# Kernel tuning notes

Hardware: AMD Instinct MI355X
Metric: run time of the kernel (lower is better)

Reference implementation:

```python
import jax, jax.numpy as jnp
import numpy as np

B, S, D = 1, 1024, 2048          # batch, seq, hidden
H, KH, HD = 16, 16, 128          # heads, kv heads, head_dim
E, K, FI = 8, 4, 1408            # experts, top_k, moe_intermediate
FS = 5632                        # shared expert intermediate
WIN = 512                        # sliding window
THETA = 1.0e6                    # rope base
EPS = 1e-6                       # rmsnorm eps


def setup_inputs() -> dict:
    key = jax.random.key(0)
    ks = jax.random.split(key, 16)
    nrm = lambda k, shape: jax.random.normal(k, shape, jnp.float32) * 0.02
    return dict(
        hidden_states=jax.random.normal(ks[0], (B, S, D), jnp.float32),
        ln1_w=jnp.ones((D,), jnp.float32),
        ln2_w=jnp.ones((D,), jnp.float32),
        wq=nrm(ks[1], (D, H * HD)), bq=jnp.zeros((H * HD,), jnp.float32),
        wk=nrm(ks[2], (D, KH * HD)), bk=jnp.zeros((KH * HD,), jnp.float32),
        wv=nrm(ks[3], (D, KH * HD)), bv=jnp.zeros((KH * HD,), jnp.float32),
        wo=nrm(ks[4], (H * HD, D)),
        w_router=nrm(ks[5], (D, E)),
        w_gate_e=nrm(ks[6], (E, D, FI)),
        w_up_e=nrm(ks[7], (E, D, FI)),
        w_down_e=nrm(ks[8], (E, FI, D)),
        ws_gate=nrm(ks[9], (D, FS)),
        ws_up=nrm(ks[10], (D, FS)),
        ws_down=nrm(ks[11], (FS, D)),
        w_shared_gate=nrm(ks[12], (D, 1)),
    )


def _rms(h, w):
    v = jnp.mean(h * h, axis=-1, keepdims=True)
    return h * jax.lax.rsqrt(v + EPS) * w


def _rope(q, k):
    pos = jnp.arange(S, dtype=jnp.float32)
    inv = 1.0 / (THETA ** (jnp.arange(0, HD, 2, dtype=jnp.float32) / HD))
    ang = pos[:, None] * inv[None, :]                      # [S, HD/2]
    cos = jnp.concatenate([jnp.cos(ang)] * 2, -1)[None, :, None, :]
    sin = jnp.concatenate([jnp.sin(ang)] * 2, -1)[None, :, None, :]
    rot = lambda t: jnp.concatenate([-t[..., HD // 2:], t[..., :HD // 2]], -1)
    return q * cos + rot(q) * sin, k * cos + rot(k) * sin


def reference(hidden_states, ln1_w, ln2_w, wq, bq, wk, bk, wv, bv, wo,
              w_router, w_gate_e, w_up_e, w_down_e,
              ws_gate, ws_up, ws_down, w_shared_gate):
    x = hidden_states
    # --- sliding-window causal attention ---
    h = _rms(x, ln1_w)
    q = (h @ wq + bq).reshape(B, S, H, HD)
    k = (h @ wk + bk).reshape(B, S, KH, HD)
    v = (h @ wv + bv).reshape(B, S, KH, HD)
    q, k = _rope(q, k)
    scores = jnp.einsum('bqhd,bkhd->bhqk', q, k) * (HD ** -0.5)
    i = jnp.arange(S)[:, None]
    j = jnp.arange(S)[None, :]
    mask = (j <= i) & (i - j < WIN)                        # causal + window
    scores = jnp.where(mask[None, None], scores, jnp.finfo(scores.dtype).min)
    attn = jax.nn.softmax(scores, axis=-1)
    o = jnp.einsum('bhqk,bkhd->bqhd', attn, v).reshape(B, S, H * HD) @ wo
    x = x + o
    # --- sparse MoE block ---
    h = _rms(x, ln2_w)
    t = h.reshape(B * S, D)
    logits = (t @ w_router).astype(jnp.float32)
    probs = jax.nn.softmax(logits, axis=-1)                # [T, E]
    top_w, top_i = jax.lax.top_k(probs, K)                 # norm_topk_prob=False
    cw = jnp.zeros((B * S, E), probs.dtype).at[jnp.arange(B * S)[:, None], top_i].set(top_w)
    # routed experts (dense combine == gather/dispatch/grouped-GEMM/combine)
    g = jnp.einsum('td,edf->etf', t, w_gate_e)
    u = jnp.einsum('td,edf->etf', t, w_up_e)
    eo = jnp.einsum('etf,efd->etd', jax.nn.silu(g) * u, w_down_e)
    routed = jnp.einsum('te,etd->td', cw, eo)
    # shared expert with sigmoid gate
    shared = (jax.nn.silu(t @ ws_gate) * (t @ ws_up)) @ ws_down
    sgate = jax.nn.sigmoid(t @ w_shared_gate)              # [T, 1]
    moe = routed + sgate * shared
    return x + moe.reshape(B, S, D)
```

## Files before the change

### kernel.cpp

```cpp
#include <hip/hip_runtime.h>

#define S_ 1024
#define D_ 2048
#define H_ 16
#define HD_ 128
#define E_ 8
#define FI_ 1408
#define FS_ 5632
#define WIN_ 512
#define T_ 1024
#define QKVN 6144

typedef _Float16 f16;
typedef __attribute__((ext_vector_type(8))) _Float16 f16x8;
typedef __attribute__((ext_vector_type(4))) _Float16 f16x4;
typedef __attribute__((ext_vector_type(4))) float f32x4;

#define MFMA16(a, b, c) __builtin_amdgcn_mfma_f32_16x16x32_f16((a), (b), (c), 0, 0, 0)

__device__ __forceinline__ void gload16(const void* g, void* l) {
    __builtin_amdgcn_global_load_lds(
        (const __attribute__((address_space(1))) unsigned*)g,
        (__attribute__((address_space(3))) unsigned*)l, 16, 0, 0);
}

__global__ __launch_bounds__(256) void rmsnorm16_kernel(const float* __restrict__ x,
                                                        const float* __restrict__ w,
                                                        f16* __restrict__ out) {
    int t = blockIdx.x;
    const float* xr = x + (long)t * D_;
    int base = threadIdx.x * 8;
    float4 v0 = *(const float4*)(xr + base);
    float4 v1 = *(const float4*)(xr + base + 4);
    float ss = v0.x*v0.x + v0.y*v0.y + v0.z*v0.z + v0.w*v0.w
             + v1.x*v1.x + v1.y*v1.y + v1.z*v1.z + v1.w*v1.w;
    #pragma unroll
    for (int off = 1; off < 64; off <<= 1) ss += __shfl_xor(ss, off);
    __shared__ float red[4];
    if ((threadIdx.x & 63) == 0) red[threadIdx.x >> 6] = ss;
    __syncthreads();
    float tot = red[0] + red[1] + red[2] + red[3];
    float scale = rsqrtf(tot / (float)D_ + 1e-6f);
    float4 w0 = *(const float4*)(w + base);
    float4 w1 = *(const float4*)(w + base + 4);
    f16x8 o;
    o[0] = (f16)(v0.x*scale*w0.x); o[1] = (f16)(v0.y*scale*w0.y);
    o[2] = (f16)(v0.z*scale*w0.z); o[3] = (f16)(v0.w*scale*w0.w);
    o[4] = (f16)(v1.x*scale*w1.x); o[5] = (f16)(v1.y*scale*w1.y);
    o[6] = (f16)(v1.z*scale*w1.z); o[7] = (f16)(v1.w*scale*w1.w);
    *(f16x8*)(out + (long)t * D_ + base) = o;
}

__global__ __launch_bounds__(256) void tconv_kernel(const float* __restrict__ src,
                                                    f16* __restrict__ dst,
                                                    int K, int N, long sSrc, long sDst,
                                                    int mode) {
    src += (long)blockIdx.z * sSrc;
    dst += (long)blockIdx.z * sDst;
    int n0 = blockIdx.x * 64, k0 = blockIdx.y * 64;
    __shared__ f16 tile[64][72];
    int t = threadIdx.x, r = t >> 2, c4 = (t & 3) * 16;
    const float* sp = src + (long)(k0 + r) * N + n0 + c4;
    #pragma unroll
    for (int i = 0; i < 16; i += 4) {
        float4 v = *(const float4*)(sp + i);
        tile[r][c4 + i + 0] = (f16)v.x; tile[r][c4 + i + 1] = (f16)v.y;
        tile[r][c4 + i + 2] = (f16)v.z; tile[r][c4 + i + 3] = (f16)v.w;
    }
    __syncthreads();
    int nr = n0 + r;
    long orow = (mode == 0) ? nr : ((long)(nr >> 4) * 32 + (nr & 15) + (mode == 2 ? 16 : 0));
    f16* dp = dst + orow * K + k0 + c4;
    #pragma unroll
    for (int i = 0; i < 16; i++) dp[i] = tile[c4 + i][r];
}

template <int EPI, int MODE>
__global__ __launch_bounds__(256) void gemm16_kernel(
    const f16* __restrict__ Ag, const f16* __restrict__ BTg,
    void* Cg, const void* auxg,
    const int* __restrict__ tokidx, const int* __restrict__ cntv,
    const float* __restrict__ tw,
    int M, int N, int K, int lda, int ldb,
    long sA, long sB, long sC) {
    int z = blockIdx.z;
    const f16* A = Ag + (long)z * sA;
    const f16* BT = BTg + (long)z * sB;
    int bm = blockIdx.y * 128, bn = blockIdx.x * 128;
    int cnt = M;
    if (MODE >= 1) {
        cnt = cntv[z];
        if (bm >= cnt) return;
    }
    int tid = threadIdx.x, lane = tid & 63, wave = tid >> 6;
    int wm = (wave >> 1) * 64, wn = (wave & 1) * 64;

    __shared__ f16 As[128][64];
    __shared__ f16 Bs[128][64];

    f32x4 acc[4][4];
    #pragma unroll
    for (int i = 0; i < 4; i++)
        #pragma unroll
        for (int j = 0; j < 4; j++) acc[i][j] = (f32x4){0.f, 0.f, 0.f, 0.f};

    int srow8 = lane >> 3;
    int scol = ((lane & 7) ^ srow8) * 8;
    const f16* Abp[4];
    const f16* Bbp[4];
    #pragma unroll
    for (int i = 0; i < 4; i++) {
        int ra = bm + wave * 32 + i * 8 + srow8;
        long arow;
        if (MODE == 1) {
            int tok = (ra < cnt) ? tokidx[z * T_ + ra] : 0;
            arow = tok;
        } else {
            arow = ra;
        }
        Abp[i] = A + arow * (long)lda + scol;
        Bbp[i] = BT + (long)(bn + wave * 32 + i * 8 + srow8) * ldb + scol;
    }

    for (int k0 = 0; k0 < K; k0 += 64) {
        __syncthreads();
        #pragma unroll
        for (int i = 0; i < 4; i++) {
            gload16(Abp[i] + k0, &As[wave * 32 + i * 8][0]);
            gload16(Bbp[i] + k0, &Bs[wave * 32 + i * 8][0]);
        }
        __syncthreads();
        #pragma unroll
        for (int kk = 0; kk < 64; kk += 32) {
            f16x8 af[4], bf[4];
            #pragma unroll
            for (int mi = 0; mi < 4; mi++) {
                int r = wm + mi * 16 + (lane & 15);
                int c = ((kk >> 3) + (lane >> 4)) ^ (r & 7);
                af[mi] = *(const f16x8*)((const char*)&As[r][0] + (c << 4));
            }
            #pragma unroll
            for (int ni = 0; ni < 4; ni++) {
                int r = wn + ni * 16 + (lane & 15);
                int c = ((kk >> 3) + (lane >> 4)) ^ (r & 7);
                bf[ni] = *(const f16x8*)((const char*)&Bs[r][0] + (c << 4));
            }
            #pragma unroll
            for (int mi = 0; mi < 4; mi++)
                #pragma unroll
                for (int ni = 0; ni < 4; ni++)
                    acc[mi][ni] = MFMA16(af[mi], bf[ni], acc[mi][ni]);
        }
    }

    if (EPI == 5) {
        int half = N >> 1;
        #pragma unroll
        for (int mi = 0; mi < 4; mi++) {
            #pragma unroll
            for (int p = 0; p < 2; p++) {
                #pragma unroll
                for (int i = 0; i < 4; i++) {
                    int m = bm + wm + mi * 16 + (lane >> 4) * 4 + i;
                    int j = ((bn + wn) >> 1) + p * 16 + (lane & 15);
                    float g = acc[mi][2 * p][i];
                    float u = acc[mi][2 * p + 1][i];
                    ((f16*)Cg + (long)z * sC)[(long)m * half + j] =
                        (f16)(g / (1.f + __expf(-g)) * u);
                }
            }
        }
        return;
    }
    #pragma unroll
    for (int mi = 0; mi < 4; mi++) {
        #pragma unroll
        for (int ni = 0; ni < 4; ni++) {
            #pragma unroll
            for (int i = 0; i < 4; i++) {
                int m = bm + wm + mi * 16 + (lane >> 4) * 4 + i;
                int n = bn + wn + ni * 16 + (lane & 15);
                long idx = (long)m * N + n;
                float v = acc[mi][ni][i];
                if (EPI == 1) {
                    ((f16*)Cg)[idx] = (f16)(v + ((const float*)auxg)[n]);
                } else if (EPI == 4) {
                    ((float*)Cg + (long)z * sC)[idx] = v;
                } else if (EPI == 6) {
                    float wv = tw[z * T_ + m];
                    ((f16*)Cg + (long)z * sC)[idx] = (f16)(v * wv);
                }
            }
        }
    }
}

__global__ __launch_bounds__(256) void rope16_kernel(f16* __restrict__ qkv) {
    int s = blockIdx.x;
    float fs = (float)s;
    for (int p = threadIdx.x; p < H_ * 64; p += 256) {
        int h = p >> 6, j = p & 63;
        float inv = __expf(-(float)j * (13.815510557964274f / 64.f));
        float ang = fs * inv;
        float c = cosf(ang), sn = sinf(ang);
        long base = (long)s * QKVN + h * HD_ + j;
        float q1 = (float)qkv[base], q2 = (float)qkv[base + 64];
        qkv[base] = (f16)(q1 * c - q2 * sn);
        qkv[base + 64] = (f16)(q2 * c + q1 * sn);
        long kb = base + 2048;
        float k1 = (float)qkv[kb], k2 = (float)qkv[kb + 64];
        qkv[kb] = (f16)(k1 * c - k2 * sn);
        qkv[kb + 64] = (f16)(k2 * c + k1 * sn);
    }
}

__global__ __launch_bounds__(256) void attn16_kernel(const f16* __restrict__ qkv,
                                                     f16* __restrict__ Og) {
    int qt = blockIdx.x * 64;
    int head = blockIdx.y;
    int tid = threadIdx.x, lane = tid & 63, wave = tid >> 6;

    __shared__ f16 Ks[64][128];
    __shared__ f16 Vrow[64][128];
    __shared__ f16 VsT[128][64];
    __shared__ f16 Ps[4][16][64];

    int qr = qt + wave * 16 + (lane & 15);
    const f16* Qp = qkv + (long)qr * QKVN + head * HD_;
    f16x8 qf[4];
    #pragma unroll
    for (int kk = 0; kk < 4; kk++)
        qf[kk] = *(const f16x8*)(Qp + kk * 32 + (lane >> 4) * 8);

    f32x4 oacc[8];
    #pragma unroll
    for (int db = 0; db < 8; db++) oacc[db] = (f32x4){0.f, 0.f, 0.f, 0.f};
    float m_run[4] = {-1e30f, -1e30f, -1e30f, -1e30f};
    float l_run[4] = {0.f, 0.f, 0.f, 0.f};

    int k_lo = qt - (WIN_ - 1);
    if (k_lo < 0) k_lo = 0;
    k_lo &= ~63;

    for (int k0 = k_lo; k0 < qt + 64; k0 += 64) {
        __syncthreads();
        {
            int row = tid >> 2, cq = (tid & 3) * 32;
            const f16* Kp = qkv + (long)(k0 + row) * QKVN + 2048 + head * HD_ + cq;
            const f16* Vp = Kp + 2048;
            #pragma unroll
            for (int u = 0; u < 32; u += 8) {
                f16x8 tk = *(const f16x8*)(Kp + u);
                int co = ((cq + u) * 2) ^ ((row & 7) << 4);
                *(f16x8*)((char*)&Ks[row][0] + co) = tk;
                *(f16x8*)(&Vrow[row][cq + u]) = *(const f16x8*)(Vp + u);
            }
        }
        __syncthreads();
        {
            int d = tid >> 1, ks = (tid & 1) * 32;
            f16 tmp[32];
            #pragma unroll
            for (int j = 0; j < 32; j++) tmp[j] = Vrow[ks + j][d];
            #pragma unroll
            for (int u = 0; u < 32; u += 8) {
                int co = ((ks + u) * 2) ^ ((d & 7) << 4);
                f16x8 tv;
                #pragma unroll
                for (int j = 0; j < 8; j++) tv[j] = tmp[u + j];
                *(f16x8*)((char*)&VsT[d][0] + co) = tv;
            }
        }
        f32x4 sacc[4];
        #pragma unroll
        for (int cb = 0; cb < 4; cb++) sacc[cb] = (f32x4){0.f, 0.f, 0.f, 0.f};
        #pragma unroll
        for (int kk = 0; kk < 4; kk++) {
            #pragma unroll
            for (int cb = 0; cb < 4; cb++) {
                int krow = cb * 16 + (lane & 15);
                int co = ((kk * 32 + (lane >> 4) * 8) * 2) ^ ((krow & 7) << 4);
                f16x8 kf = *(const f16x8*)((const char*)&Ks[krow][0] + co);
                sacc[cb] = MFMA16(qf[kk], kf, sacc[cb]);
            }
        }
        float mtile[4] = {-1e30f, -1e30f, -1e30f, -1e30f};
        #pragma unroll
        for (int cb = 0; cb < 4; cb++) {
            #pragma unroll
            for (int i = 0; i < 4; i++) {
                int qi = qt + wave * 16 + (lane >> 4) * 4 + i;
                int kj = k0 + cb * 16 + (lane & 15);
                float s = sacc[cb][i] * 0.08838834764831845f;
                bool valid = (kj <= qi) && (qi - kj < WIN_);
                s = valid ? s : -1e30f;
                sacc[cb][i] = s;
                mtile[i] = fmaxf(mtile[i], s);
            }
        }
        #pragma unroll
        for (int i = 0; i < 4; i++) {
            float v = mtile[i];
            v = fmaxf(v, __shfl_xor(v, 1));
            v = fmaxf(v, __shfl_xor(v, 2));
            v = fmaxf(v, __shfl_xor(v, 4));
            v = fmaxf(v, __shfl_xor(v, 8));
            mtile[i] = v;
        }
        float pscale[4], lsum[4];
        #pragma unroll
        for (int i = 0; i < 4; i++) {
            float mnew = fmaxf(m_run[i], mtile[i]);
            pscale[i] = __expf(m_run[i] - mnew);
            m_run[i] = mnew;
            lsum[i] = 0.f;
        }
        #pragma unroll
        for (int cb = 0; cb < 4; cb++) {
            #pragma unroll
            for (int i = 0; i < 4; i++) {
                float mn = fmaxf(m_run[i], -1e20f);
                float p = __expf(sacc[cb][i] - mn);
                lsum[i] += p;
                int prow = (lane >> 4) * 4 + i;
                int pcol = cb * 16 + (lane & 15);
                int co = (pcol * 2) ^ ((prow & 7) << 4);
                *(f16*)((char*)&Ps[wave][prow][0] + co) = (f16)p;
            }
        }
        #pragma unroll
        for (int i = 0; i < 4; i++) {
            float v = lsum[i];
            v += __shfl_xor(v, 1);
            v += __shfl_xor(v, 2);
            v += __shfl_xor(v, 4);
            v += __shfl_xor(v, 8);
            l_run[i] = l_run[i] * pscale[i] + v;
        }
        #pragma unroll
        for (int db = 0; db < 8; db++)
            #pragma unroll
            for (int i = 0; i < 4; i++) oacc[db][i] *= pscale[i];
        __syncthreads();
        #pragma unroll
        for (int ks = 0; ks < 2; ks++) {
            int prow = lane & 15;
            int co = ((ks * 32 + (lane >> 4) * 8) * 2) ^ ((prow & 7) << 4);
            f16x8 pf = *(const f16x8*)((const char*)&Ps[wave][prow][0] + co);
            #pragma unroll
            for (int db = 0; db < 8; db++) {
                int vrow2 = db * 16 + (lane & 15);
                int co2 = ((ks * 32 + (lane >> 4) * 8) * 2) ^ ((vrow2 & 7) << 4);
                f16x8 vf = *(const f16x8*)((const char*)&VsT[vrow2][0] + co2);
                oacc[db] = MFMA16(pf, vf, oacc[db]);
            }
        }
    }
    #pragma unroll
    for (int db = 0; db < 8; db++) {
        #pragma unroll
        for (int i = 0; i < 4; i++) {
            int qi = qt + wave * 16 + (lane >> 4) * 4 + i;
            int d = db * 16 + (lane & 15);
            Og[(long)qi * D_ + head * HD_ + d] = (f16)(oacc[db][i] / l_run[i]);
        }
    }
}

__global__ __launch_bounds__(256) void router_kernel(
    const float* __restrict__ x2, const float* __restrict__ ln2,
    const float* __restrict__ wr, const float* __restrict__ wshg,
    float* __restrict__ cw, float* __restrict__ sgate) {
    int t = blockIdx.x;
    const float* xr = x2 + (long)t * D_;
    int base = threadIdx.x * 8;
    float xv[8];
    *(float4*)&xv[0] = *(const float4*)(xr + base);
    *(float4*)&xv[4] = *(const float4*)(xr + base + 4);
    float ss = 0.f;
    #pragma unroll
    for (int j = 0; j < 8; j++) ss += xv[j] * xv[j];
    #pragma unroll
    for (int off = 1; off < 64; off <<= 1) ss += __shfl_xor(ss, off);
    __shared__ float red0[4];
    if ((threadIdx.x & 63) == 0) red0[threadIdx.x >> 6] = ss;
    __syncthreads();
    float scale = rsqrtf((red0[0] + red0[1] + red0[2] + red0[3]) / (float)D_ + 1e-6f);

    float part[9] = {0.f,0.f,0.f,0.f,0.f,0.f,0.f,0.f,0.f};
    #pragma unroll
    for (int j = 0; j < 8; j++) {
        int d = base + j;
        float hv = xv[j] * scale * ln2[d];
        const float* wrow = wr + (long)d * E_;
        #pragma unroll
        for (int e = 0; e < 8; e++) part[e] += hv * wrow[e];
        part[8] += hv * wshg[d];
    }
    #pragma unroll
    for (int e = 0; e < 9; e++) {
        float v = part[e];
        #pragma unroll
        for (int off = 1; off < 64; off <<= 1) v += __shfl_xor(v, off);
        part[e] = v;
    }
    __shared__ float red[4][9];
    int lane = threadIdx.x & 63, wave = threadIdx.x >> 6;
    if (lane == 0)
        #pragma unroll
        for (int e = 0; e < 9; e++) red[wave][e] = part[e];
    __syncthreads();
    if (threadIdx.x == 0) {
        float logit[9];
        #pragma unroll
        for (int e = 0; e < 9; e++) logit[e] = red[0][e] + red[1][e] + red[2][e] + red[3][e];
        float mx = logit[0];
        #pragma unroll
        for (int e = 1; e < 8; e++) mx = fmaxf(mx, logit[e]);
        float p[8], sum = 0.f;
        #pragma unroll
        for (int e = 0; e < 8; e++) { p[e] = expf(logit[e] - mx); sum += p[e]; }
        #pragma unroll
        for (int e = 0; e < 8; e++) p[e] /= sum;
        float sel[8] = {0.f,0.f,0.f,0.f,0.f,0.f,0.f,0.f};
        float tmp[8];
        #pragma unroll
        for (int e = 0; e < 8; e++) tmp[e] = p[e];
        for (int it = 0; it < 4; it++) {
            int best = 0;
            float bvv = tmp[0];
            #pragma unroll
            for (int e = 1; e < 8; e++)
                if (tmp[e] > bvv) { bvv = tmp[e]; best = e; }
            sel[best] = p[best];
            tmp[best] = -1.f;
        }
        #pragma unroll
        for (int e = 0; e < 8; e++) cw[(long)e * T_ + t] = sel[e];
        sgate[t] = 1.f / (1.f + expf(-logit[8]));
    }
}

__global__ __launch_bounds__(512) void bucket_kernel(const float* __restrict__ cw,
                                                     int* __restrict__ cnt,
                                                     int* __restrict__ tokidx,
                                                     float* __restrict__ tw,
                                                     int* __restrict__ posmat) {
    int e = threadIdx.x >> 6, lane = threadIdx.x & 63;
    int count = 0;
    for (int base = 0; base < T_; base += 64) {
        int t = base + lane;
        float wv = cw[(long)e * T_ + t];
        unsigned long long m = __ballot(wv > 0.f);
        int pre = __popcll(m & ((1ull << lane) - 1ull));
        if (wv > 0.f) {
            int s = count + pre;
            tokidx[e * T_ + s] = t;
            tw[e * T_ + s] = wv;
            posmat[e * T_ + t] = s;
        }
        count += __popcll(m);
    }
    if (lane == 0) cnt[e] = count;
}

__global__ __launch_bounds__(256) void biascat_kernel(const float* bq, const float* bk,
                                                      const float* bv, float* bqkv) {
    int i = blockIdx.x * 256 + threadIdx.x;
    if (i < 2048) bqkv[i] = bq[i];
    else if (i < 4096) bqkv[i] = bk[i - 2048];
    else if (i < 6144) bqkv[i] = bv[i - 4096];
}

__global__ __launch_bounds__(256) void reduce2r_kernel(const float* __restrict__ x,
                                                       const float* __restrict__ p,
                                                       float* __restrict__ out) {
    long total = (long)T_ * D_ / 4;
    for (long i = (long)blockIdx.x * 256 + threadIdx.x; i < total;
         i += (long)gridDim.x * 256) {
        float4 a = ((const float4*)x)[i];
        float4 b = ((const float4*)p)[i];
        float4 c = ((const float4*)p)[i + total];
        float4 o;
        o.x = a.x + b.x + c.x; o.y = a.y + b.y + c.y;
        o.z = a.z + b.z + c.z; o.w = a.w + b.w + c.w;
        ((float4*)out)[i] = o;
    }
}

__global__ __launch_bounds__(256) void reduce4_kernel(const float* __restrict__ p,
                                                      float* __restrict__ out) {
    long total = (long)T_ * D_ / 4;
    for (long i = (long)blockIdx.x * 256 + threadIdx.x; i < total;
         i += (long)gridDim.x * 256) {
        float4 a = ((const float4*)p)[i];
        float4 b = ((const float4*)p)[i + total];
        float4 c = ((const float4*)p)[i + 2 * total];
        float4 d = ((const float4*)p)[i + 3 * total];
        float4 o;
        o.x = a.x + b.x + c.x + d.x; o.y = a.y + b.y + c.y + d.y;
        o.z = a.z + b.z + c.z + d.z; o.w = a.w + b.w + c.w + d.w;
        ((float4*)out)[i] = o;
    }
}

__global__ __launch_bounds__(256) void combine_kernel(
    const float* __restrict__ x2, const float* __restrict__ sho,
    const float* __restrict__ sg, const float* __restrict__ cw,
    const int* __restrict__ posmat, const f16* __restrict__ eo,
    float* __restrict__ out) {
    long total = (long)T_ * D_ / 4;
    for (long i = (long)blockIdx.x * 256 + threadIdx.x; i < total;
         i += (long)gridDim.x * 256) {
        int t = (int)(i >> 9);
        int c4 = (int)(i & 511) * 4;
        float4 a = ((const float4*)x2)[i];
        float4 s = ((const float4*)sho)[i];
        float g = sg[t];
        float r0 = a.x + g * s.x, r1 = a.y + g * s.y;
        float r2 = a.z + g * s.z, r3 = a.w + g * s.w;
        #pragma unroll
        for (int e = 0; e < 8; e++) {
            float w = cw[(long)e * T_ + t];
            if (w > 0.f) {
                int slot = posmat[(long)e * T_ + t];
                f16x4 v = *(const f16x4*)(eo + ((long)e * T_ + slot) * D_ + c4);
                r0 += (float)v[0]; r1 += (float)v[1];
                r2 += (float)v[2]; r3 += (float)v[3];
            }
        }
        float4 o; o.x = r0; o.y = r1; o.z = r2; o.w = r3;
        ((float4*)out)[i] = o;
    }
}

extern "C" void kernel_launch(void* const* d_in, const int* in_sizes, int n_in,
                              void* d_out, int out_size, void* d_ws, size_t ws_size,
                              hipStream_t stream) {
    const float* x    = (const float*)d_in[0];
    const float* ln1  = (const float*)d_in[1];
    const float* ln2  = (const float*)d_in[2];
    const float* wq   = (const float*)d_in[3];
    const float* bq   = (const float*)d_in[4];
    const float* wk   = (const float*)d_in[5];
    const float* bk   = (const float*)d_in[6];
    const float* wv   = (const float*)d_in[7];
    const float* bv   = (const float*)d_in[8];
    const float* wo   = (const float*)d_in[9];
    const float* wrt  = (const float*)d_in[10];
    const float* wge  = (const float*)d_in[11];
    const float* wue  = (const float*)d_in[12];
    const float* wde  = (const float*)d_in[13];
    const float* wsg  = (const float*)d_in[14];
    const float* wsu  = (const float*)d_in[15];
    const float* wsd  = (const float*)d_in[16];
    const float* wshg = (const float*)d_in[17];

    float* ws = (float*)d_ws;
    f16*   wT     = (f16*)ws;
    float* x2     = ws + 11534336;
    float* sho    = x2 + 2097152;
    float* bqkv   = sho + 2097152;
    float* cw     = bqkv + 6144;
    float* sg     = cw + 8192;
    int*   cnt    = (int*)(sg + 1024);
    int*   tokidx = cnt + 8;
    float* tw     = (float*)(tokidx + 8192);
    int*   posmat = (int*)(tw + 8192);
    f16*   h1     = (f16*)(posmat + 8192);
    f16*   h2     = (f16*)((float*)h1 + 1048576);
    float* pool   = (float*)h2 + 1048576;

    f16*   qkv     = (f16*)pool;
    float* woparts = pool + 3145728;
    f16*   sgb     = (f16*)pool;
    float* parts4  = pool + 2883584;
    f16*   Gg      = (f16*)pool;
    f16*   eo      = (f16*)(pool + 5767168);
    f16*   ao      = h1;

    dim3 blk(256);

    rmsnorm16_kernel<<<T_, blk, 0, stream>>>(x, ln1, h1);
    biascat_kernel<<<24, blk, 0, stream>>>(bq, bk, bv, bqkv);
    tconv_kernel<<<dim3(32, 32, 1), blk, 0, stream>>>(wq, wT, 2048, 2048, 0, 0, 0);
    tconv_kernel<<<dim3(32, 32, 1), blk, 0, stream>>>(wk, wT + 2048L * 2048, 2048, 2048, 0, 0, 0);
    tconv_kernel<<<dim3(32, 32, 1), blk, 0, stream>>>(wv, wT + 4096L * 2048, 2048, 2048, 0, 0, 0);
    gemm16_kernel<1, 0><<<dim3(48, 8, 1), blk, 0, stream>>>(
        h1, wT, qkv, bqkv, nullptr, nullptr, nullptr,
        T_, QKVN, D_, 2048, 2048, 0, 0, 0);
    rope16_kernel<<<S_, blk, 0, stream>>>(qkv);
    attn16_kernel<<<dim3(16, 16), blk, 0, stream>>>(qkv, ao);
    tconv_kernel<<<dim3(32, 32, 1), blk, 0, stream>>>(wo, wT, 2048, 2048, 0, 0, 0);
    gemm16_kernel<4, 0><<<dim3(16, 8, 2), blk, 0, stream>>>(
        ao, wT, woparts, nullptr, nullptr, nullptr, nullptr,
        T_, D_, 1024, 2048, 2048, 1024, 1024, 2097152);
    reduce2r_kernel<<<512, blk, 0, stream>>>(x, woparts, x2);

    rmsnorm16_kernel<<<T_, blk, 0, stream>>>(x2, ln2, h2);
    router_kernel<<<T_, blk, 0, stream>>>(x2, ln2, wrt, wshg, cw, sg);
    bucket_kernel<<<1, 512, 0, stream>>>(cw, cnt, tokidx, tw, posmat);

    tconv_kernel<<<dim3(88, 32, 1), blk, 0, stream>>>(wsg, wT, 2048, 5632, 0, 0, 1);
    tconv_kernel<<<dim3(88, 32, 1), blk, 0, stream>>>(wsu, wT, 2048, 5632, 0, 0, 2);
    gemm16_kernel<5, 0><<<dim3(88, 8, 1), blk, 0, stream>>>(
        h2, wT, sgb, nullptr, nullptr, nullptr, nullptr,
        T_, 2 * FS_, D_, 2048, 2048, 0, 0, 0);
    tconv_kernel<<<dim3(32, 88, 1), blk, 0, stream>>>(wsd, wT, 5632, 2048, 0, 0, 0);
    gemm16_kernel<4, 0><<<dim3(16, 8, 4), blk, 0, stream>>>(
        sgb, wT, parts4, nullptr, nullptr, nullptr, nullptr,
        T_, D_, 1408, 5632, 5632, 1408, 1408, 2097152);
    reduce4_kernel<<<512, blk, 0, stream>>>(parts4, sho);

    tconv_kernel<<<dim3(22, 32, 4), blk, 0, stream>>>(wge, wT, 2048, 1408,
                                                      2048L * 1408, 2816L * 2048, 1);
    tconv_kernel<<<dim3(22, 32, 4), blk, 0, stream>>>(wue, wT, 2048, 1408,
                                                      2048L * 1408, 2816L * 2048, 2);
    gemm16_kernel<5, 1><<<dim3(22, 8, 4), blk, 0, stream>>>(
        h2, wT, Gg, nullptr, tokidx, cnt, nullptr,
        T_, 2 * FI_, D_, 2048, 2048, 0, 2816L * 2048, 1024L * 1408);
    tconv_kernel<<<dim3(22, 32, 4), blk, 0, stream>>>(wge + 4L * 2048 * 1408, wT, 2048, 1408,
                                                      2048L * 1408, 2816L * 2048, 1);
    tconv_kernel<<<dim3(22, 32, 4), blk, 0, stream>>>(wue + 4L * 2048 * 1408, wT, 2048, 1408,
                                                      2048L * 1408, 2816L * 2048, 2);
    gemm16_kernel<5, 1><<<dim3(22, 8, 4), blk, 0, stream>>>(
        h2, wT, Gg + 4L * 1024 * 1408, nullptr, tokidx + 4 * T_, cnt + 4, nullptr,
        T_, 2 * FI_, D_, 2048, 2048, 0, 2816L * 2048, 1024L * 1408);

    tconv_kernel<<<dim3(32, 22, 4), blk, 0, stream>>>(wde, wT, 1408, 2048,
                                                      1408L * 2048, 2048L * 1408, 0);
    gemm16_kernel<6, 2><<<dim3(16, 8, 4), blk, 0, stream>>>(
        Gg, wT, eo, nullptr, nullptr, cnt, tw,
        T_, D_, 1408, 1408, 1408, 1024L * 1408, 2048L * 1408, 1024L * 2048);
    tconv_kernel<<<dim3(32, 22, 4), blk, 0, stream>>>(wde + 4L * 1408 * 2048, wT, 1408, 2048,
                                                      1408L * 2048, 2048L * 1408, 0);
    gemm16_kernel<6, 2><<<dim3(16, 8, 4), blk, 0, stream>>>(
        Gg + 4L * 1024 * 1408, wT, eo + 4L * 1024 * 2048, nullptr, nullptr, cnt + 4, tw + 4 * T_,
        T_, D_, 1408, 1408, 1408, 1024L * 1408, 2048L * 1408, 1024L * 2048);

    combine_kernel<<<1024, blk, 0, stream>>>(x2, sho, sg, cw, posmat, eo, (float*)d_out);
}
```

Baseline: 603.3 us.

## Fuse residual add, rmsnorm and router; vectorize transpose stores; merge gate/up converts

The two-way residual reduction, second rmsnorm and router are merged into one per-token kernel that writes x2, the fp16 h2 and the routing weights, so x2 is not re-read from global memory twice. The weight transpose-convert kernel now transposes while writing to shared memory and emits 16-byte vector global stores instead of scalar 2-byte stores. Gate and up weight conversions are merged into one launch each, using the z dimension, which cuts the launch count. The transposed shared-memory writes may now hit bank conflicts.

```diff
diff --git a/kernel.cpp b/kernel.cpp
--- a/kernel.cpp
+++ b/kernel.cpp
@@ -51,12 +51,9 @@
     *(f16x8*)(out + (long)t * D_ + base) = o;
 }
 
-__global__ __launch_bounds__(256) void tconv_kernel(const float* __restrict__ src,
-                                                    f16* __restrict__ dst,
-                                                    int K, int N, long sSrc, long sDst,
-                                                    int mode) {
-    src += (long)blockIdx.z * sSrc;
-    dst += (long)blockIdx.z * sDst;
+__device__ __forceinline__ void tconv_body(const float* __restrict__ src,
+                                           f16* __restrict__ dst,
+                                           int K, int N, int mode) {
     int n0 = blockIdx.x * 64, k0 = blockIdx.y * 64;
     __shared__ f16 tile[64][72];
     int t = threadIdx.x, r = t >> 2, c4 = (t & 3) * 16;
@@ -64,15 +61,39 @@
     #pragma unroll
     for (int i = 0; i < 16; i += 4) {
         float4 v = *(const float4*)(sp + i);
-        tile[r][c4 + i + 0] = (f16)v.x; tile[r][c4 + i + 1] = (f16)v.y;
-        tile[r][c4 + i + 2] = (f16)v.z; tile[r][c4 + i + 3] = (f16)v.w;
+        tile[c4 + i + 0][r] = (f16)v.x;
+        tile[c4 + i + 1][r] = (f16)v.y;
+        tile[c4 + i + 2][r] = (f16)v.z;
+        tile[c4 + i + 3][r] = (f16)v.w;
     }
     __syncthreads();
-    int nr = n0 + r;
-    long orow = (mode == 0) ? nr : ((long)(nr >> 4) * 32 + (nr & 15) + (mode == 2 ? 16 : 0));
-    f16* dp = dst + orow * K + k0 + c4;
-    #pragma unroll
-    for (int i = 0; i < 16; i++) dp[i] = tile[c4 + i][r];
+    #pragma unroll
+    for (int h = 0; h < 2; h++) {
+        int v = t + h * 256;
+        int nl = v >> 3, c8 = (v & 7) * 8;
+        f16x8 vec = *(const f16x8*)&tile[nl][c8];
+        int nr = n0 + nl;
+        long orow = (mode == 0) ? nr
+                  : ((long)(nr >> 4) * 32 + (nr & 15) + (mode == 2 ? 16 : 0));
+        *(f16x8*)(dst + orow * K + k0 + c8) = vec;
+    }
+}
+
+__global__ __launch_bounds__(256) void tconv_kernel(const float* __restrict__ src,
+                                                    f16* __restrict__ dst,
+                                                    int K, int N, long sSrc, long sDst) {
+    tconv_body(src + (long)blockIdx.z * sSrc, dst + (long)blockIdx.z * sDst, K, N, 0);
+}
+
+__global__ __launch_bounds__(256) void tconv_gu_kernel(const float* __restrict__ srcA,
+                                                       const float* __restrict__ srcB,
+                                                       f16* __restrict__ dst,
+                                                       int K, int N, long sSrc, long sDst,
+                                                       int zsplit) {
+    int z = blockIdx.z;
+    int e = (z < zsplit) ? z : z - zsplit;
+    const float* src = ((z < zsplit) ? srcA : srcB) + (long)e * sSrc;
+    tconv_body(src, dst + (long)e * sDst, K, N, (z < zsplit) ? 1 : 2);
 }
 
 template <int EPI, int MODE>
@@ -367,16 +388,30 @@
     }
 }
 
-__global__ __launch_bounds__(256) void router_kernel(
-    const float* __restrict__ x2, const float* __restrict__ ln2,
-    const float* __restrict__ wr, const float* __restrict__ wshg,
+__global__ __launch_bounds__(256) void postattn_kernel(
+    const float* __restrict__ x, const float* __restrict__ p,
+    const float* __restrict__ ln2, const float* __restrict__ wr,
+    const float* __restrict__ wshg,
+    float* __restrict__ x2, f16* __restrict__ h2,
     float* __restrict__ cw, float* __restrict__ sgate) {
     int t = blockIdx.x;
-    const float* xr = x2 + (long)t * D_;
     int base = threadIdx.x * 8;
+    long ro = (long)t * D_ + base;
+    const long plane = (long)T_ * D_;
     float xv[8];
-    *(float4*)&xv[0] = *(const float4*)(xr + base);
-    *(float4*)&xv[4] = *(const float4*)(xr + base + 4);
+    #pragma unroll
+    for (int j = 0; j < 8; j += 4) {
+        float4 a = *(const float4*)(x + ro + j);
+        float4 b = *(const float4*)(p + ro + j);
+        float4 c = *(const float4*)(p + plane + ro + j);
+        xv[j + 0] = a.x + b.x + c.x;
+        xv[j + 1] = a.y + b.y + c.y;
+        xv[j + 2] = a.z + b.z + c.z;
+        xv[j + 3] = a.w + b.w + c.w;
+    }
+    *(float4*)(x2 + ro) = *(float4*)&xv[0];
+    *(float4*)(x2 + ro + 4) = *(float4*)&xv[4];
+
     float ss = 0.f;
     #pragma unroll
     for (int j = 0; j < 8; j++) ss += xv[j] * xv[j];
@@ -388,15 +423,19 @@
     float scale = rsqrtf((red0[0] + red0[1] + red0[2] + red0[3]) / (float)D_ + 1e-6f);
 
     float part[9] = {0.f,0.f,0.f,0.f,0.f,0.f,0.f,0.f,0.f};
+    f16x8 ho;
     #pragma unroll
     for (int j = 0; j < 8; j++) {
         int d = base + j;
         float hv = xv[j] * scale * ln2[d];
+        ho[j] = (f16)hv;
         const float* wrow = wr + (long)d * E_;
         #pragma unroll
         for (int e = 0; e < 8; e++) part[e] += hv * wrow[e];
         part[8] += hv * wshg[d];
     }
+    *(f16x8*)(h2 + ro) = ho;
+
     #pragma unroll
     for (int e = 0; e < 9; e++) {
         float v = part[e];
@@ -417,22 +456,22 @@
         float mx = logit[0];
         #pragma unroll
         for (int e = 1; e < 8; e++) mx = fmaxf(mx, logit[e]);
-        float p[8], sum = 0.f;
-        #pragma unroll
-        for (int e = 0; e < 8; e++) { p[e] = expf(logit[e] - mx); sum += p[e]; }
-        #pragma unroll
-        for (int e = 0; e < 8; e++) p[e] /= sum;
+        float pp[8], sum = 0.f;
+        #pragma unroll
+        for (int e = 0; e < 8; e++) { pp[e] = expf(logit[e] - mx); sum += pp[e]; }
+        #pragma unroll
+        for (int e = 0; e < 8; e++) pp[e] /= sum;
         float sel[8] = {0.f,0.f,0.f,0.f,0.f,0.f,0.f,0.f};
         float tmp[8];
         #pragma unroll
-        for (int e = 0; e < 8; e++) tmp[e] = p[e];
+        for (int e = 0; e < 8; e++) tmp[e] = pp[e];
         for (int it = 0; it < 4; it++) {
             int best = 0;
             float bvv = tmp[0];
             #pragma unroll
             for (int e = 1; e < 8; e++)
                 if (tmp[e] > bvv) { bvv = tmp[e]; best = e; }
-            sel[best] = p[best];
+            sel[best] = pp[best];
             tmp[best] = -1.f;
         }
         #pragma unroll
@@ -470,22 +509,6 @@
     if (i < 2048) bqkv[i] = bq[i];
     else if (i < 4096) bqkv[i] = bk[i - 2048];
     else if (i < 6144) bqkv[i] = bv[i - 4096];
-}
-
-__global__ __launch_bounds__(256) void reduce2r_kernel(const float* __restrict__ x,
-                                                       const float* __restrict__ p,
-                                                       float* __restrict__ out) {
-    long total = (long)T_ * D_ / 4;
-    for (long i = (long)blockIdx.x * 256 + threadIdx.x; i < total;
-         i += (long)gridDim.x * 256) {
-        float4 a = ((const float4*)x)[i];
-        float4 b = ((const float4*)p)[i];
-        float4 c = ((const float4*)p)[i + total];
-        float4 o;
-        o.x = a.x + b.x + c.x; o.y = a.y + b.y + c.y;
-        o.z = a.z + b.z + c.z; o.w = a.w + b.w + c.w;
-        ((float4*)out)[i] = o;
-    }
 }
 
 __global__ __launch_bounds__(256) void reduce4_kernel(const float* __restrict__ p,
@@ -583,57 +606,50 @@
 
     rmsnorm16_kernel<<<T_, blk, 0, stream>>>(x, ln1, h1);
     biascat_kernel<<<24, blk, 0, stream>>>(bq, bk, bv, bqkv);
-    tconv_kernel<<<dim3(32, 32, 1), blk, 0, stream>>>(wq, wT, 2048, 2048, 0, 0, 0);
-    tconv_kernel<<<dim3(32, 32, 1), blk, 0, stream>>>(wk, wT + 2048L * 2048, 2048, 2048, 0, 0, 0);
-    tconv_kernel<<<dim3(32, 32, 1), blk, 0, stream>>>(wv, wT + 4096L * 2048, 2048, 2048, 0, 0, 0);
+    tconv_kernel<<<dim3(32, 32, 1), blk, 0, stream>>>(wq, wT, 2048, 2048, 0, 0);
+    tconv_kernel<<<dim3(32, 32, 1), blk, 0, stream>>>(wk, wT + 2048L * 2048, 2048, 2048, 0, 0);
+    tconv_kernel<<<dim3(32, 32, 1), blk, 0, stream>>>(wv, wT + 4096L * 2048, 2048, 2048, 0, 0);
     gemm16_kernel<1, 0><<<dim3(48, 8, 1), blk, 0, stream>>>(
         h1, wT, qkv, bqkv, nullptr, nullptr, nullptr,
         T_, QKVN, D_, 2048, 2048, 0, 0, 0);
     rope16_kernel<<<S_, blk, 0, stream>>>(qkv);
     attn16_kernel<<<dim3(16, 16), blk, 0, stream>>>(qkv, ao);
-    tconv_kernel<<<dim3(32, 32, 1), blk, 0, stream>>>(wo, wT, 2048, 2048, 0, 0, 0);
+    tconv_kernel<<<dim3(32, 32, 1), blk, 0, stream>>>(wo, wT, 2048, 2048, 0, 0);
     gemm16_kernel<4, 0><<<dim3(16, 8, 2), blk, 0, stream>>>(
         ao, wT, woparts, nullptr, nullptr, nullptr, nullptr,
         T_, D_, 1024, 2048, 2048, 1024, 1024, 2097152);
-    reduce2r_kernel<<<512, blk, 0, stream>>>(x, woparts, x2);
-
-    rmsnorm16_kernel<<<T_, blk, 0, stream>>>(x2, ln2, h2);
-    router_kernel<<<T_, blk, 0, stream>>>(x2, ln2, wrt, wshg, cw, sg);
+    postattn_kernel<<<T_, blk, 0, stream>>>(x, woparts, ln2, wrt, wshg, x2, h2, cw, sg);
     bucket_kernel<<<1, 512, 0, stream>>>(cw, cnt, tokidx, tw, posmat);
 
-    tconv_kernel<<<dim3(88, 32, 1), blk, 0, stream>>>(wsg, wT, 2048, 5632, 0, 0, 1);
-    tconv_kernel<<<dim3(88, 32, 1), blk, 0, stream>>>(wsu, wT, 2048, 5632, 0, 0, 2);
+    tconv_gu_kernel<<<dim3(88, 32, 2), blk, 0, stream>>>(wsg, wsu, wT, 2048, 5632, 0, 0, 1);
     gemm16_kernel<5, 0><<<dim3(88, 8, 1), blk, 0, stream>>>(
         h2, wT, sgb, nullptr, nullptr, nullptr, nullptr,
         T_, 2 * FS_, D_, 2048, 2048, 0, 0, 0);
-    tconv_kernel<<<dim3(32, 88, 1), blk, 0, stream>>>(wsd, wT, 5632, 2048, 0, 0, 0);
+    tconv_kernel<<<dim3(32, 88, 1), blk, 0, stream>>>(wsd, wT, 5632, 2048, 0, 0);
     gemm16_kernel<4, 0><<<dim3(16, 8, 4), blk, 0, stream>>>(
         sgb, wT, parts4, nullptr, nullptr, nullptr, nullptr,
         T_, D_, 1408, 5632, 5632, 1408, 1408, 2097152);
     reduce4_kernel<<<512, blk, 0, stream>>>(parts4, sho);
 
-    tconv_kernel<<<dim3(22, 32, 4), blk, 0, stream>>>(wge, wT, 2048, 1408,
-                                                      2048L * 1408, 2816L * 2048, 1);
-    tconv_kernel<<<dim3(22, 32, 4), blk, 0, stream>>>(wue, wT, 2048, 1408,
-                                                      2048L * 1408, 2816L * 2048, 2);
+    tconv_gu_kernel<<<dim3(22, 32, 8), blk, 0, stream>>>(
+        wge, wue, wT, 2048, 1408, 2048L * 1408, 2816L * 2048, 4);
     gemm16_kernel<5, 1><<<dim3(22, 8, 4), blk, 0, stream>>>(
         h2, wT, Gg, nullptr, tokidx, cnt, nullptr,
         T_, 2 * FI_, D_, 2048, 2048, 0, 2816L * 2048, 1024L * 1408);
-    tconv_kernel<<<dim3(22, 32, 4), blk, 0, stream>>>(wge + 4L * 2048 * 1408, wT, 2048, 1408,
-                                                      2048L * 1408, 2816L * 2048, 1);
-    tconv_kernel<<<dim3(22, 32, 4), blk, 0, stream>>>(wue + 4L * 2048 * 1408, wT, 2048, 1408,
-                                                      2048L * 1408, 2816L * 2048, 2);
+    tconv_gu_kernel<<<dim3(22, 32, 8), blk, 0, stream>>>(
+        wge + 4L * 2048 * 1408, wue + 4L * 2048 * 1408, wT, 2048, 1408,
+        2048L * 1408, 2816L * 2048, 4);
     gemm16_kernel<5, 1><<<dim3(22, 8, 4), blk, 0, stream>>>(
         h2, wT, Gg + 4L * 1024 * 1408, nullptr, tokidx + 4 * T_, cnt + 4, nullptr,
         T_, 2 * FI_, D_, 2048, 2048, 0, 2816L * 2048, 1024L * 1408);
 
     tconv_kernel<<<dim3(32, 22, 4), blk, 0, stream>>>(wde, wT, 1408, 2048,
-                                                      1408L * 2048, 2048L * 1408, 0);
+                                                      1408L * 2048, 2048L * 1408);
     gemm16_kernel<6, 2><<<dim3(16, 8, 4), blk, 0, stream>>>(
         Gg, wT, eo, nullptr, nullptr, cnt, tw,
         T_, D_, 1408, 1408, 1408, 1024L * 1408, 2048L * 1408, 1024L * 2048);
     tconv_kernel<<<dim3(32, 22, 4), blk, 0, stream>>>(wde + 4L * 1408 * 2048, wT, 1408, 2048,
-                                                      1408L * 2048, 2048L * 1408, 0);
+                                                      1408L * 2048, 2048L * 1408);
     gemm16_kernel<6, 2><<<dim3(16, 8, 4), blk, 0, stream>>>(
         Gg + 4L * 1024 * 1408, wT, eo + 4L * 1024 * 2048, nullptr, nullptr, cnt + 4, tw + 4 * T_,
         T_, D_, 1408, 1408, 1408, 1024L * 1408, 2048L * 1408, 1024L * 2048);
```

Result: faster. 578.4 us (-4.1%).
